# Kernel tuning notes

Measured on AMD Instinct MI355X. Metric: run time of the kernel, lower is better.

## Reference

```python
import jax, jax.numpy as jnp
import numpy as np

N = 10000        # nodes
E = 160000       # edges (before self loops)
F_IN = 4         # n_features
D = 128          # d_model (per-head out channels for GAT, GCN width)
H = 8            # n_heads
NEG_SLOPE = 0.2  # PyG GATConv default leaky relu slope


def setup_inputs() -> dict:
    key = jax.random.key(0)
    ks = jax.random.split(key, 10)
    x = jax.random.normal(ks[0], (N, F_IN), dtype=jnp.float32)
    edge_index = jax.random.randint(ks[1], (2, E), 0, N, dtype=jnp.int64)
    s = 0.05
    gat_w = jax.random.normal(ks[2], (F_IN, H * D), dtype=jnp.float32) * s
    att_src = jax.random.normal(ks[3], (H, D), dtype=jnp.float32) * s
    att_dst = jax.random.normal(ks[4], (H, D), dtype=jnp.float32) * s
    gat_b = jnp.zeros((H * D,), dtype=jnp.float32)
    gcn1_w = jax.random.normal(ks[5], (H * D, D), dtype=jnp.float32) * s
    gcn1_b = jnp.zeros((D,), dtype=jnp.float32)
    gcn2_w = jax.random.normal(ks[6], (D, D), dtype=jnp.float32) * s
    gcn2_b = jnp.zeros((D,), dtype=jnp.float32)
    return {"x": x, "edge_index": edge_index, "gat_w": gat_w,
            "att_src": att_src, "att_dst": att_dst, "gat_b": gat_b,
            "gcn1_w": gcn1_w, "gcn1_b": gcn1_b,
            "gcn2_w": gcn2_w, "gcn2_b": gcn2_b}


def _add_self_loops(edge_index, n):
    loops = jnp.arange(n, dtype=edge_index.dtype)
    src = jnp.concatenate([edge_index[0], loops])
    dst = jnp.concatenate([edge_index[1], loops])
    return src, dst


def _gat_conv(x, src, dst, w, att_src, att_dst, b):
    # PyG GATConv, concat=True: h [N,H,D]
    h = (x @ w).reshape(-1, H, D)
    a_s = jnp.einsum('nhd,hd->nh', h, att_src)   # per-node src score
    a_d = jnp.einsum('nhd,hd->nh', h, att_dst)   # per-node dst score
    e = jax.nn.leaky_relu(a_s[src] + a_d[dst], NEG_SLOPE)  # [Etot,H]
    # segment softmax over destination node, per head
    m = jax.ops.segment_max(e, dst, num_segments=N)
    ex = jnp.exp(e - m[dst])
    denom = jax.ops.segment_sum(ex, dst, num_segments=N)
    alpha = ex / denom[dst]                       # [Etot,H]
    msg = h[src] * alpha[:, :, None]              # [Etot,H,D]
    out = jax.ops.segment_sum(msg, dst, num_segments=N)  # [N,H,D]
    return out.reshape(-1, H * D) + b


def _gcn_conv(x, src, dst, w, b):
    # PyG GCNConv with symmetric normalization (self loops already added)
    h = x @ w
    deg = jax.ops.segment_sum(jnp.ones_like(dst, dtype=h.dtype), dst,
                              num_segments=N)
    dinv = jnp.where(deg > 0, jax.lax.rsqrt(deg), 0.0)
    norm = dinv[src] * dinv[dst]                  # [Etot]
    out = jax.ops.segment_sum(h[src] * norm[:, None], dst, num_segments=N)
    return out + b


def reference(x, edge_index, gat_w, att_src, att_dst, gat_b,
              gcn1_w, gcn1_b, gcn2_w, gcn2_b):
    src, dst = _add_self_loops(edge_index, N)
    h = _gat_conv(x, src, dst, gat_w, att_src, att_dst, gat_b)
    h = jax.nn.gelu(h, approximate=False)         # torch F.gelu is exact erf
    h = _gcn_conv(h, src, dst, gcn1_w, gcn1_b)
    h = jax.nn.gelu(h, approximate=False)
    h = _gcn_conv(h, src, dst, gcn2_w, gcn2_b)
    return h                                      # [N, D]
```

## Files before the change

kernel.cpp:

```cpp
#include <hip/hip_runtime.h>
#include <math.h>

#define HEADS 8
#define DHEAD 128
#define CMODEL 1024
#define BCAP 64

typedef __attribute__((ext_vector_type(8))) short bf16x8;
typedef __attribute__((ext_vector_type(4))) float f32x4;

__device__ __forceinline__ float gelu_exact(float x) {
    return 0.5f * x * (1.0f + erff(x * 0.70710678118654752440f));
}

__device__ __forceinline__ unsigned short f2bf(float f) {
    unsigned u = __float_as_uint(f);
    return (unsigned short)((u + 0x7FFFu + ((u >> 16) & 1u)) >> 16);
}
__device__ __forceinline__ float bf2f(unsigned short h) {
    return __uint_as_float((unsigned)h << 16);
}

__global__ void __launch_bounds__(256) k_scores(const float* __restrict__ x,
                                                const float* __restrict__ gat_w,
                                                const float* __restrict__ att_src,
                                                const float* __restrict__ att_dst,
                                                const float* __restrict__ W1,
                                                const float* __restrict__ W2,
                                                float* __restrict__ xpack,
                                                float* __restrict__ a_d,
                                                int* __restrict__ cursor,
                                                unsigned short* __restrict__ W1hi,
                                                unsigned short* __restrict__ W1lo,
                                                unsigned short* __restrict__ W2hi,
                                                unsigned short* __restrict__ W2lo,
                                                int n_nodes, int nb_scores) {
    if ((int)blockIdx.x >= nb_scores) {
        int t = (blockIdx.x - nb_scores) * 256 + threadIdx.x;
        const int total1 = (1024 >> 5) * 8 * 64;
        const int total2 = (128 >> 5) * 8 * 64;
        const float* W; unsigned short *Whi, *Wlo;
        if (t < total1) { W = W1; Whi = W1hi; Wlo = W1lo; }
        else if (t < total1 + total2) { t -= total1; W = W2; Whi = W2hi; Wlo = W2lo; }
        else return;
        int lane = t & 63;
        int ct = (t >> 6) & 7;
        int kc = t >> 9;
        int quad = lane >> 4;
        int col = ct * 16 + (lane & 15);
        size_t o = (size_t)t * 8;
        #pragma unroll
        for (int j = 0; j < 8; j++) {
            float w = W[(size_t)(kc * 32 + quad * 8 + j) * 128 + col];
            unsigned short h = f2bf(w);
            Whi[o + j] = h;
            Wlo[o + j] = f2bf(w - bf2f(h));
        }
        return;
    }
    __shared__ float ws_s[32], ws_d[32];
    int t = threadIdx.x;
    if (t < 64) {
        int e = t >> 1;
        int which = t & 1;
        int hh = e >> 2, k = e & 3;
        const float* wrow = gat_w + k * CMODEL + hh * DHEAD;
        const float* av = which ? (att_dst + hh * DHEAD) : (att_src + hh * DHEAD);
        float s = 0.0f;
        for (int c = 0; c < DHEAD; c++) s += wrow[c] * av[c];
        if (which) ws_d[e] = s; else ws_s[e] = s;
    }
    int gid = blockIdx.x * 256 + t;
    if (gid < n_nodes) cursor[gid] = 0;
    __syncthreads();
    int p = gid;
    if (p >= n_nodes * HEADS) return;
    int n = p >> 3, hh = p & 7;
    float4 xv = *(const float4*)(x + (size_t)n * 4);
    float4 ws = *(const float4*)&ws_s[hh * 4];
    float4 wd = *(const float4*)&ws_d[hh * 4];
    a_d[p] = xv.x * wd.x + xv.y * wd.y + xv.z * wd.z + xv.w * wd.w;
    xpack[(size_t)n * 16 + 4 + hh] =
        xv.x * ws.x + xv.y * ws.y + xv.z * ws.z + xv.w * ws.w;
    if (hh == 0) *(float4*)(xpack + (size_t)n * 16) = xv;
}

__global__ void __launch_bounds__(256) k_scatter(const int* __restrict__ ei,
                                                 int* __restrict__ cursor,
                                                 int* __restrict__ bucket,
                                                 int n_nodes, int n_edges) {
    int e = blockIdx.x * 256 + threadIdx.x;
    int etot = n_edges + n_nodes;
    if (e >= etot) return;
    int s, d;
    if (e < n_edges) { s = ei[e]; d = ei[n_edges + e]; }
    else             { s = d = e - n_edges; }
    int pos = atomicAdd(&cursor[d], 1);
    if (pos < BCAP) bucket[(d << 6) + pos] = s;
}

__global__ void __launch_bounds__(256, 3) k_smax_mm1(const float* __restrict__ xpack,
                                                  const float* __restrict__ a_d,
                                                  const int* __restrict__ deg,
                                                  const int* __restrict__ bucket,
                                                  const float* __restrict__ gat_w,
                                                  const float* __restrict__ gat_b,
                                                  const unsigned short* __restrict__ Bhi,
                                                  const unsigned short* __restrict__ Blo,
                                                  float* __restrict__ t,
                                                  int n_nodes) {
    __shared__ float xs[16 * 32];
    __shared__ float ck[2][16 * 68];
    int mb = blockIdx.x;
    int tid = threadIdx.x;
    int lane = tid & 63;
    int w = tid >> 6;

    bf16x8 bhA[2][2], blA[2][2], bhB[2][2], blB[2][2];
    #pragma unroll
    for (int kc2 = 0; kc2 < 2; kc2++)
        #pragma unroll
        for (int ct = 0; ct < 2; ct++) {
            size_t bi = (((size_t)(kc2 * 8) + w * 2 + ct) * 64 + lane) * 8;
            bhA[kc2][ct] = *(const bf16x8*)(Bhi + bi);
            blA[kc2][ct] = *(const bf16x8*)(Blo + bi);
        }

    {
        int q = tid >> 1;
        int half = tid & 1;
        int ln = tid >> 4, hh = q & 7;
        int n = mb * 16 + ln;
        int nc = (n < n_nodes) ? n : (n_nodes - 1);
        int grp = lane & 48;
        int gl = lane & 15;
        int basec = nc << 6;
        int pre0 = bucket[basec + gl];
        int pre1 = bucket[basec + 16 + gl];
        int pre2 = bucket[basec + 32 + gl];
        int pre3 = bucket[basec + 48 + gl];
        auto SRC = [&](int e) -> int {
            int v = (e < 16) ? pre0 : (e < 32) ? pre1 : (e < 48) ? pre2 : pre3;
            return __shfl(v, grp + (e & 15), 64);
        };
        float sum = 0.0f;
        float4 acc = make_float4(0, 0, 0, 0);
        if (n < n_nodes) {
            int dg = deg[n]; if (dg > BCAP) dg = BCAP;
            float ad = a_d[n * 8 + hh];
            int r = half;
            for (; r + 6 < dg; r += 8) {
                int s0 = SRC(r + 0), s1 = SRC(r + 2);
                int s2 = SRC(r + 4), s3 = SRC(r + 6);
                const float* p0 = xpack + (size_t)s0 * 16;
                const float* p1 = xpack + (size_t)s1 * 16;
                const float* p2 = xpack + (size_t)s2 * 16;
                const float* p3 = xpack + (size_t)s3 * 16;
                float e0 = p0[4 + hh] + ad, e1 = p1[4 + hh] + ad;
                float e2 = p2[4 + hh] + ad, e3 = p3[4 + hh] + ad;
                float4 x0 = *(const float4*)p0;
                float4 x1 = *(const float4*)p1;
                float4 x2 = *(const float4*)p2;
                float4 x3 = *(const float4*)p3;
                e0 = (e0 > 0.0f) ? e0 : 0.2f * e0;  float w0 = __expf(e0);
                e1 = (e1 > 0.0f) ? e1 : 0.2f * e1;  float w1 = __expf(e1);
                e2 = (e2 > 0.0f) ? e2 : 0.2f * e2;  float w2 = __expf(e2);
                e3 = (e3 > 0.0f) ? e3 : 0.2f * e3;  float w3 = __expf(e3);
                sum += w0 + w1 + w2 + w3;
                acc.x += w0 * x0.x + w1 * x1.x + w2 * x2.x + w3 * x3.x;
                acc.y += w0 * x0.y + w1 * x1.y + w2 * x2.y + w3 * x3.y;
                acc.z += w0 * x0.z + w1 * x1.z + w2 * x2.z + w3 * x3.z;
                acc.w += w0 * x0.w + w1 * x1.w + w2 * x2.w + w3 * x3.w;
            }
            for (; r < dg; r += 2) {
                int s = SRC(r);
                const float* ps = xpack + (size_t)s * 16;
                float e = ps[4 + hh] + ad;
                e = (e > 0.0f) ? e : 0.2f * e;
                float ex = __expf(e);
                float4 xv = *(const float4*)ps;
                sum += ex;
                acc.x += ex * xv.x; acc.y += ex * xv.y;
                acc.z += ex * xv.z; acc.w += ex * xv.w;
            }
        }
        sum   += __shfl_down(sum, 1);
        acc.x += __shfl_down(acc.x, 1);
        acc.y += __shfl_down(acc.y, 1);
        acc.z += __shfl_down(acc.z, 1);
        acc.w += __shfl_down(acc.w, 1);
        if (half == 0) {
            float inv = (sum > 0.0f) ? (1.0f / sum) : 0.0f;
            *(float4*)&xs[q * 4] = make_float4(acc.x * inv, acc.y * inv,
                                               acc.z * inv, acc.w * inv);
        }
    }
    __syncthreads();

    int lm = lane & 15, quad = lane >> 4;
    int cc = tid & 63;
    int rp = tid >> 6;
    f32x4 macc[2];
    macc[0] = (f32x4){0.0f, 0.0f, 0.0f, 0.0f};
    macc[1] = (f32x4){0.0f, 0.0f, 0.0f, 0.0f};

#define ROUND(RR, BH, BL, BH_N, BL_N, RNEXT)                                    \
    {                                                                           \
        int buf = (RR) & 1;                                                     \
        int col = (RR) * 64 + cc;                                               \
        float w0 = gat_w[col], w1 = gat_w[1024 + col],                          \
              w2 = gat_w[2048 + col], w3 = gat_w[3072 + col];                   \
        float bb = gat_b[col];                                                  \
        int hh2 = (RR) >> 1;                                                    \
        _Pragma("unroll")                                                       \
        for (int rr = 0; rr < 4; rr++) {                                        \
            int row = rp * 4 + rr;                                              \
            float4 xa = *(const float4*)&xs[(row * 8 + hh2) * 4];               \
            float v = xa.x * w0 + xa.y * w1 + xa.z * w2 + xa.w * w3 + bb;       \
            ck[buf][row * 68 + cc] = gelu_exact(v);                             \
        }                                                                       \
        _Pragma("unroll")                                                       \
        for (int kc2 = 0; kc2 < 2; kc2++)                                       \
            _Pragma("unroll")                                                   \
            for (int ct = 0; ct < 2; ct++) {                                    \
                size_t bi = (((size_t)((RNEXT) * 2 + kc2) * 8 + w * 2 + ct) * 64 + lane) * 8; \
                BH_N[kc2][ct] = *(const bf16x8*)(Bhi + bi);                     \
                BL_N[kc2][ct] = *(const bf16x8*)(Blo + bi);                     \
            }                                                                   \
        asm volatile("s_waitcnt lgkmcnt(0)" ::: "memory");                      \
        __builtin_amdgcn_s_barrier();                                           \
        __builtin_amdgcn_sched_barrier(0);                                      \
        _Pragma("unroll")                                                       \
        for (int kc2 = 0; kc2 < 2; kc2++) {                                     \
            float a[8];                                                         \
            *(float4*)&a[0] = *(const float4*)&ck[buf][lm * 68 + kc2 * 32 + quad * 8];     \
            *(float4*)&a[4] = *(const float4*)&ck[buf][lm * 68 + kc2 * 32 + quad * 8 + 4]; \
            bf16x8 ah, al;                                                      \
            _Pragma("unroll")                                                   \
            for (int j = 0; j < 8; j++) {                                       \
                unsigned short h = f2bf(a[j]);                                  \
                ah[j] = (short)h;                                               \
                al[j] = (short)f2bf(a[j] - bf2f(h));                            \
            }                                                                   \
            _Pragma("unroll")                                                   \
            for (int ct = 0; ct < 2; ct++) {                                    \
                macc[ct] = __builtin_amdgcn_mfma_f32_16x16x32_bf16(ah, BH[kc2][ct], macc[ct], 0, 0, 0); \
                macc[ct] = __builtin_amdgcn_mfma_f32_16x16x32_bf16(al, BH[kc2][ct], macc[ct], 0, 0, 0); \
                macc[ct] = __builtin_amdgcn_mfma_f32_16x16x32_bf16(ah, BL[kc2][ct], macc[ct], 0, 0, 0); \
            }                                                                   \
        }                                                                       \
    }

    for (int r = 0; r < 16; r += 2) {
        ROUND(r,     bhA, blA, bhB, blB, r + 1);
        ROUND(r + 1, bhB, blB, bhA, blA, (r + 2 < 16 ? r + 2 : 15));
    }
#undef ROUND

    #pragma unroll
    for (int ct = 0; ct < 2; ct++) {
        int col = (w * 2 + ct) * 16 + lm;
        #pragma unroll
        for (int reg = 0; reg < 4; reg++) {
            int row = mb * 16 + quad * 4 + reg;
            if (row < n_nodes) {
                float dv = 1.0f / sqrtf((float)deg[row]);
                t[(size_t)row * 128 + col] = macc[ct][reg] * dv;
            }
        }
    }
}

__global__ void __launch_bounds__(512) k_gcn1_fused(const float* __restrict__ t,
                                                    const int* __restrict__ deg,
                                                    const int* __restrict__ bucket,
                                                    const float* __restrict__ bias,
                                                    const unsigned short* __restrict__ Bhi,
                                                    const unsigned short* __restrict__ Blo,
                                                    float* __restrict__ t2,
                                                    int n_nodes) {
    __shared__ float hs[16][132];
    int tid = threadIdx.x;
    int mb = blockIdx.x;
    int c = tid & 31;
    int ln = tid >> 5;
    int node = mb * 16 + ln;
    int nc = (node < n_nodes) ? node : (n_nodes - 1);
    int base = nc << 6;
    int sa = bucket[base + c];
    int sb = bucket[base + 32 + c];
    int dgt = (node < n_nodes) ? deg[node] : 1;
    int dg = dgt > BCAP ? BCAP : dgt;
    float dn = 1.0f / sqrtf((float)dgt);
    int d1 = dg > 32 ? 32 : dg;
    #pragma unroll
    for (int h2 = 0; h2 < 2; h2++) {
        const float* tp = t + h2 * 64 + c * 2;
        float2 acc = make_float2(0.0f, 0.0f);
        int r = 0;
        for (; r + 4 <= d1; r += 4) {
            int s0 = __shfl(sa, r + 0, 32);
            int s1 = __shfl(sa, r + 1, 32);
            int s2 = __shfl(sa, r + 2, 32);
            int s3 = __shfl(sa, r + 3, 32);
            float2 v0 = *(const float2*)(tp + (size_t)s0 * 128);
            float2 v1 = *(const float2*)(tp + (size_t)s1 * 128);
            float2 v2 = *(const float2*)(tp + (size_t)s2 * 128);
            float2 v3 = *(const float2*)(tp + (size_t)s3 * 128);
            acc.x += v0.x + v1.x + v2.x + v3.x;
            acc.y += v0.y + v1.y + v2.y + v3.y;
        }
        for (; r < d1; r++) {
            int s = __shfl(sa, r, 32);
            float2 v = *(const float2*)(tp + (size_t)s * 128);
            acc.x += v.x; acc.y += v.y;
        }
        for (; r < dg; r++) {
            int s = __shfl(sb, r - 32, 32);
            float2 v = *(const float2*)(tp + (size_t)s * 128);
            acc.x += v.x; acc.y += v.y;
        }
        int k = h2 * 64 + c * 2;
        float2 bb = *(const float2*)(bias + k);
        hs[ln][k]     = gelu_exact(acc.x * dn + bb.x);
        hs[ln][k + 1] = gelu_exact(acc.y * dn + bb.y);
    }
    __syncthreads();
    int lane = tid & 63;
    int w = tid >> 6;
    int lm = lane & 15, quad = lane >> 4;
    f32x4 acc2 = (f32x4){0.0f, 0.0f, 0.0f, 0.0f};
    #pragma unroll
    for (int kc = 0; kc < 4; kc++) {
        float a[8];
        *(float4*)&a[0] = *(const float4*)&hs[lm][kc * 32 + quad * 8];
        *(float4*)&a[4] = *(const float4*)&hs[lm][kc * 32 + quad * 8 + 4];
        bf16x8 ah, al;
        #pragma unroll
        for (int j = 0; j < 8; j++) {
            unsigned short h = f2bf(a[j]);
            ah[j] = (short)h;
            al[j] = (short)f2bf(a[j] - bf2f(h));
        }
        bf16x8 bh = *(const bf16x8*)(Bhi + (((size_t)(kc * 8 + w)) * 64 + lane) * 8);
        bf16x8 bl = *(const bf16x8*)(Blo + (((size_t)(kc * 8 + w)) * 64 + lane) * 8);
        acc2 = __builtin_amdgcn_mfma_f32_16x16x32_bf16(ah, bh, acc2, 0, 0, 0);
        acc2 = __builtin_amdgcn_mfma_f32_16x16x32_bf16(al, bh, acc2, 0, 0, 0);
        acc2 = __builtin_amdgcn_mfma_f32_16x16x32_bf16(ah, bl, acc2, 0, 0, 0);
    }
    int col = w * 16 + lm;
    #pragma unroll
    for (int reg = 0; reg < 4; reg++) {
        int row = mb * 16 + quad * 4 + reg;
        if (row < n_nodes) {
            float dv = 1.0f / sqrtf((float)deg[row]);
            t2[(size_t)row * 128 + col] = acc2[reg] * dv;
        }
    }
}

__global__ void __launch_bounds__(256) k_gcn_agg(const float* __restrict__ t,
                                                 const int* __restrict__ deg,
                                                 const int* __restrict__ bucket,
                                                 const float* __restrict__ bias,
                                                 float* __restrict__ outF,
                                                 int n_nodes) {
    int c = threadIdx.x & 31;
    int ln = threadIdx.x >> 5;
    int n = blockIdx.x * 8 + ln;
    int col0 = blockIdx.y * 64;
    if (n >= n_nodes) return;
    float2 acc = make_float2(0.0f, 0.0f);
    int dgt = deg[n];
    int dg = dgt > BCAP ? BCAP : dgt;
    int base = n << 6;
    int sa = bucket[base + c];
    int sb = bucket[base + 32 + c];
    const float* tp = t + col0 + c * 2;
    int d1 = dg > 32 ? 32 : dg;
    int r = 0;
    for (; r + 4 <= d1; r += 4) {
        int s0 = __shfl(sa, r + 0, 32);
        int s1 = __shfl(sa, r + 1, 32);
        int s2 = __shfl(sa, r + 2, 32);
        int s3 = __shfl(sa, r + 3, 32);
        float2 v0 = *(const float2*)(tp + (size_t)s0 * 128);
        float2 v1 = *(const float2*)(tp + (size_t)s1 * 128);
        float2 v2 = *(const float2*)(tp + (size_t)s2 * 128);
        float2 v3 = *(const float2*)(tp + (size_t)s3 * 128);
        acc.x += v0.x + v1.x + v2.x + v3.x;
        acc.y += v0.y + v1.y + v2.y + v3.y;
    }
    for (; r < d1; r++) {
        int s = __shfl(sa, r, 32);
        float2 v = *(const float2*)(tp + (size_t)s * 128);
        acc.x += v.x; acc.y += v.y;
    }
    for (; r < dg; r++) {
        int s = __shfl(sb, r - 32, 32);
        float2 v = *(const float2*)(tp + (size_t)s * 128);
        acc.x += v.x; acc.y += v.y;
    }
    float dn = 1.0f / sqrtf((float)dgt);
    int k = col0 + c * 2;
    float2 bb = *(const float2*)(bias + k);
    *(float2*)(outF + (size_t)n * 128 + k) =
        make_float2(acc.x * dn + bb.x, acc.y * dn + bb.y);
}

extern "C" void kernel_launch(void* const* d_in, const int* in_sizes, int n_in,
                              void* d_out, int out_size, void* d_ws, size_t ws_size,
                              hipStream_t stream) {
    const float* x        = (const float*)d_in[0];
    const int*   ei       = (const int*)d_in[1];
    const float* gat_w    = (const float*)d_in[2];
    const float* att_src  = (const float*)d_in[3];
    const float* att_dst  = (const float*)d_in[4];
    const float* gat_b    = (const float*)d_in[5];
    const float* gcn1_w   = (const float*)d_in[6];
    const float* gcn1_b   = (const float*)d_in[7];
    const float* gcn2_w   = (const float*)d_in[8];
    const float* gcn2_b   = (const float*)d_in[9];
    float* out = (float*)d_out;

    int N = in_sizes[0] / 4;
    int E = in_sizes[1] / 2;
    int Etot = E + N;
    int n_mtiles = (N + 15) / 16;

    char* base = (char*)d_ws;
    float*          t      = (float*)(base);
    float*          t2     = (float*)(base + 5120000);
    unsigned short* w1hi   = (unsigned short*)(base + 26000000);
    unsigned short* w1lo   = (unsigned short*)(base + 26262144);
    unsigned short* w2hi   = (unsigned short*)(base + 26524288);
    unsigned short* w2lo   = (unsigned short*)(base + 26557056);
    size_t off = 81920000;
    float* xpack  = (float*)(base + off); off += (size_t)N * 16 * 4;
    float* a_d    = (float*)(base + off); off += (size_t)N * 8 * 4;
    int*   cursor = (int*)(base + off);   off += (size_t)N * 4;
    int*   bucket = (int*)(base + off);   off += (size_t)N * BCAP * 4;

    int nb_scores = (N * HEADS + 255) / 256;
    int nb_wswz   = (16384 + 2048 + 255) / 256;

    k_scores<<<nb_scores + nb_wswz, 256, 0, stream>>>(x, gat_w, att_src, att_dst,
                                                      gcn1_w, gcn2_w, xpack, a_d, cursor,
                                                      w1hi, w1lo, w2hi, w2lo, N, nb_scores);

    k_scatter<<<(Etot + 255) / 256, 256, 0, stream>>>(ei, cursor, bucket, N, E);

    k_smax_mm1<<<n_mtiles, 256, 0, stream>>>(xpack, a_d, cursor, bucket,
                                             gat_w, gat_b, w1hi, w1lo, t, N);

    k_gcn1_fused<<<n_mtiles, 512, 0, stream>>>(t, cursor, bucket, gcn1_b,
                                               w2hi, w2lo, t2, N);

    k_gcn_agg<<<dim3((N + 7) / 8, 2), 256, 0, stream>>>(t2, cursor, bucket, gcn2_b,
                                                        out, N);
}
```

Measured before the change: 153.1 us.

## Double k_smax_mm1 block to 512 threads, one column tile per wave

Changes the fused GAT softmax-aggregation plus GEMM kernel from 256 to 512 threads per block. Each wave now owns one 16-column MFMA tile instead of two, and four lanes instead of two split each node-head's edge loop, with an extra shuffle reduction. This cuts per-thread register pressure and serial work to raise occupancy and latency hiding. In exchange it adds shuffle overhead and larger-block barrier synchronisation.

```diff
diff --git a/kernel.cpp b/kernel.cpp
--- a/kernel.cpp
+++ b/kernel.cpp
@@ -99,7 +99,7 @@
     if (pos < BCAP) bucket[(d << 6) + pos] = s;
 }
 
-__global__ void __launch_bounds__(256, 3) k_smax_mm1(const float* __restrict__ xpack,
+__global__ void __launch_bounds__(512, 4) k_smax_mm1(const float* __restrict__ xpack,
                                                   const float* __restrict__ a_d,
                                                   const int* __restrict__ deg,
                                                   const int* __restrict__ bucket,
@@ -116,42 +116,38 @@
     int lane = tid & 63;
     int w = tid >> 6;
 
-    bf16x8 bhA[2][2], blA[2][2], bhB[2][2], blB[2][2];
+    bf16x8 bhA[2], blA[2], bhB[2], blB[2];
     #pragma unroll
-    for (int kc2 = 0; kc2 < 2; kc2++)
-        #pragma unroll
-        for (int ct = 0; ct < 2; ct++) {
-            size_t bi = (((size_t)(kc2 * 8) + w * 2 + ct) * 64 + lane) * 8;
-            bhA[kc2][ct] = *(const bf16x8*)(Bhi + bi);
-            blA[kc2][ct] = *(const bf16x8*)(Blo + bi);
-        }
+    for (int kc2 = 0; kc2 < 2; kc2++) {
+        size_t bi = (((size_t)kc2 * 8 + w) * 64 + lane) * 8;
+        bhA[kc2] = *(const bf16x8*)(Bhi + bi);
+        blA[kc2] = *(const bf16x8*)(Blo + bi);
+    }
 
     {
-        int q = tid >> 1;
-        int half = tid & 1;
-        int ln = tid >> 4, hh = q & 7;
+        int ln = tid >> 5;
+        int g = tid & 31;
+        int hh = g >> 2;
+        int quarter = g & 3;
         int n = mb * 16 + ln;
         int nc = (n < n_nodes) ? n : (n_nodes - 1);
-        int grp = lane & 48;
-        int gl = lane & 15;
         int basec = nc << 6;
-        int pre0 = bucket[basec + gl];
-        int pre1 = bucket[basec + 16 + gl];
-        int pre2 = bucket[basec + 32 + gl];
-        int pre3 = bucket[basec + 48 + gl];
+        int sa = bucket[basec + g];
+        int sb = bucket[basec + 32 + g];
+        int grp = lane & 32;
         auto SRC = [&](int e) -> int {
-            int v = (e < 16) ? pre0 : (e < 32) ? pre1 : (e < 48) ? pre2 : pre3;
-            return __shfl(v, grp + (e & 15), 64);
+            int v = (e < 32) ? sa : sb;
+            return __shfl(v, grp + (e & 31), 64);
         };
         float sum = 0.0f;
         float4 acc = make_float4(0, 0, 0, 0);
         if (n < n_nodes) {
             int dg = deg[n]; if (dg > BCAP) dg = BCAP;
             float ad = a_d[n * 8 + hh];
-            int r = half;
-            for (; r + 6 < dg; r += 8) {
-                int s0 = SRC(r + 0), s1 = SRC(r + 2);
-                int s2 = SRC(r + 4), s3 = SRC(r + 6);
+            int r = quarter;
+            for (; r + 12 < dg; r += 16) {
+                int s0 = SRC(r + 0), s1 = SRC(r + 4);
+                int s2 = SRC(r + 8), s3 = SRC(r + 12);
                 const float* p0 = xpack + (size_t)s0 * 16;
                 const float* p1 = xpack + (size_t)s1 * 16;
                 const float* p2 = xpack + (size_t)s2 * 16;
@@ -172,7 +168,7 @@
                 acc.z += w0 * x0.z + w1 * x1.z + w2 * x2.z + w3 * x3.z;
                 acc.w += w0 * x0.w + w1 * x1.w + w2 * x2.w + w3 * x3.w;
             }
-            for (; r < dg; r += 2) {
+            for (; r < dg; r += 4) {
                 int s = SRC(r);
                 const float* ps = xpack + (size_t)s * 16;
                 float e = ps[4 + hh] + ad;
@@ -189,10 +185,15 @@
         acc.y += __shfl_down(acc.y, 1);
         acc.z += __shfl_down(acc.z, 1);
         acc.w += __shfl_down(acc.w, 1);
-        if (half == 0) {
+        sum   += __shfl_down(sum, 2);
+        acc.x += __shfl_down(acc.x, 2);
+        acc.y += __shfl_down(acc.y, 2);
+        acc.z += __shfl_down(acc.z, 2);
+        acc.w += __shfl_down(acc.w, 2);
+        if (quarter == 0) {
             float inv = (sum > 0.0f) ? (1.0f / sum) : 0.0f;
-            *(float4*)&xs[q * 4] = make_float4(acc.x * inv, acc.y * inv,
-                                               acc.z * inv, acc.w * inv);
+            *(float4*)&xs[(ln * 8 + hh) * 4] = make_float4(acc.x * inv, acc.y * inv,
+                                                           acc.z * inv, acc.w * inv);
         }
     }
     __syncthreads();
@@ -200,9 +201,7 @@
     int lm = lane & 15, quad = lane >> 4;
     int cc = tid & 63;
     int rp = tid >> 6;
-    f32x4 macc[2];
-    macc[0] = (f32x4){0.0f, 0.0f, 0.0f, 0.0f};
-    macc[1] = (f32x4){0.0f, 0.0f, 0.0f, 0.0f};
+    f32x4 macc = (f32x4){0.0f, 0.0f, 0.0f, 0.0f};
 
 #define ROUND(RR, BH, BL, BH_N, BL_N, RNEXT)                                    \
     {                                                                           \
@@ -213,20 +212,18 @@
         float bb = gat_b[col];                                                  \
         int hh2 = (RR) >> 1;                                                    \
         _Pragma("unroll")                                                       \
-        for (int rr = 0; rr < 4; rr++) {                                        \
-            int row = rp * 4 + rr;                                              \
+        for (int rr = 0; rr < 2; rr++) {                                        \
+            int row = rp * 2 + rr;                                              \
             float4 xa = *(const float4*)&xs[(row * 8 + hh2) * 4];               \
             float v = xa.x * w0 + xa.y * w1 + xa.z * w2 + xa.w * w3 + bb;       \
             ck[buf][row * 68 + cc] = gelu_exact(v);                             \
         }                                                                       \
         _Pragma("unroll")                                                       \
-        for (int kc2 = 0; kc2 < 2; kc2++)                                       \
-            _Pragma("unroll")                                                   \
-            for (int ct = 0; ct < 2; ct++) {                                    \
-                size_t bi = (((size_t)((RNEXT) * 2 + kc2) * 8 + w * 2 + ct) * 64 + lane) * 8; \
-                BH_N[kc2][ct] = *(const bf16x8*)(Bhi + bi);                     \
-                BL_N[kc2][ct] = *(const bf16x8*)(Blo + bi);                     \
-            }                                                                   \
+        for (int kc2 = 0; kc2 < 2; kc2++) {                                     \
+            size_t bi = (((size_t)((RNEXT) * 2 + kc2) * 8 + w) * 64 + lane) * 8;\
+            BH_N[kc2] = *(const bf16x8*)(Bhi + bi);                             \
+            BL_N[kc2] = *(const bf16x8*)(Blo + bi);                             \
+        }                                                                       \
         asm volatile("s_waitcnt lgkmcnt(0)" ::: "memory");                      \
         __builtin_amdgcn_s_barrier();                                           \
         __builtin_amdgcn_sched_barrier(0);                                      \
@@ -242,12 +239,9 @@
                 ah[j] = (short)h;                                               \
                 al[j] = (short)f2bf(a[j] - bf2f(h));                            \
             }                                                                   \
-            _Pragma("unroll")                                                   \
-            for (int ct = 0; ct < 2; ct++) {                                    \
-                macc[ct] = __builtin_amdgcn_mfma_f32_16x16x32_bf16(ah, BH[kc2][ct], macc[ct], 0, 0, 0); \
-                macc[ct] = __builtin_amdgcn_mfma_f32_16x16x32_bf16(al, BH[kc2][ct], macc[ct], 0, 0, 0); \
-                macc[ct] = __builtin_amdgcn_mfma_f32_16x16x32_bf16(ah, BL[kc2][ct], macc[ct], 0, 0, 0); \
-            }                                                                   \
+            macc = __builtin_amdgcn_mfma_f32_16x16x32_bf16(ah, BH[kc2], macc, 0, 0, 0); \
+            macc = __builtin_amdgcn_mfma_f32_16x16x32_bf16(al, BH[kc2], macc, 0, 0, 0); \
+            macc = __builtin_amdgcn_mfma_f32_16x16x32_bf16(ah, BL[kc2], macc, 0, 0, 0); \
         }                                                                       \
     }
 
@@ -257,15 +251,14 @@
     }
 #undef ROUND
 
-    #pragma unroll
-    for (int ct = 0; ct < 2; ct++) {
-        int col = (w * 2 + ct) * 16 + lm;
+    {
+        int col = w * 16 + lm;
         #pragma unroll
         for (int reg = 0; reg < 4; reg++) {
             int row = mb * 16 + quad * 4 + reg;
             if (row < n_nodes) {
                 float dv = 1.0f / sqrtf((float)deg[row]);
-                t[(size_t)row * 128 + col] = macc[ct][reg] * dv;
+                t[(size_t)row * 128 + col] = macc[reg] * dv;
             }
         }
     }
@@ -450,7 +443,7 @@
 
     k_scatter<<<(Etot + 255) / 256, 256, 0, stream>>>(ei, cursor, bucket, N, E);
 
-    k_smax_mm1<<<n_mtiles, 256, 0, stream>>>(xpack, a_d, cursor, bucket,
+    k_smax_mm1<<<n_mtiles, 512, 0, stream>>>(xpack, a_d, cursor, bucket,
                                              gat_w, gat_b, w1hi, w1lo, t, N);
 
     k_gcn1_fused<<<n_mtiles, 512, 0, stream>>>(t, cursor, bucket, gcn1_b,
```

Result: slower. 162.0 us (+5.8%).

## Split GEMM K-dimension across waves with LDS reduction in smax_mm1

Applied to the files above, without the earlier changes.

Replaces the column-split MFMA loop, which staged GELU activations through a double-buffered LDS tile with a barrier every round, with a split-K scheme. Each wave computes GELU activations for its own K slices directly in registers and accumulates all 128 output columns. The four partial sums are then reduced through shared memory before the scaled write. This removes the 16 per-round barriers and the LDS round trip for activations, but needs more accumulator registers. The launch-bounds occupancy hint is dropped and a serial reduction by one wave is added.

```diff
diff --git a/kernel.cpp b/kernel.cpp
--- a/kernel.cpp
+++ b/kernel.cpp
@@ -99,7 +99,7 @@
     if (pos < BCAP) bucket[(d << 6) + pos] = s;
 }
 
-__global__ void __launch_bounds__(256, 3) k_smax_mm1(const float* __restrict__ xpack,
+__global__ void __launch_bounds__(256) k_smax_mm1(const float* __restrict__ xpack,
                                                   const float* __restrict__ a_d,
                                                   const int* __restrict__ deg,
                                                   const int* __restrict__ bucket,
@@ -110,21 +110,11 @@
                                                   float* __restrict__ t,
                                                   int n_nodes) {
     __shared__ float xs[16 * 32];
-    __shared__ float ck[2][16 * 68];
+    __shared__ float red[3][64][36];
     int mb = blockIdx.x;
     int tid = threadIdx.x;
     int lane = tid & 63;
     int w = tid >> 6;
-
-    bf16x8 bhA[2][2], blA[2][2], bhB[2][2], blB[2][2];
-    #pragma unroll
-    for (int kc2 = 0; kc2 < 2; kc2++)
-        #pragma unroll
-        for (int ct = 0; ct < 2; ct++) {
-            size_t bi = (((size_t)(kc2 * 8) + w * 2 + ct) * 64 + lane) * 8;
-            bhA[kc2][ct] = *(const bf16x8*)(Bhi + bi);
-            blA[kc2][ct] = *(const bf16x8*)(Blo + bi);
-        }
 
     {
         int q = tid >> 1;
@@ -198,74 +188,71 @@
     __syncthreads();
 
     int lm = lane & 15, quad = lane >> 4;
-    int cc = tid & 63;
-    int rp = tid >> 6;
-    f32x4 macc[2];
-    macc[0] = (f32x4){0.0f, 0.0f, 0.0f, 0.0f};
-    macc[1] = (f32x4){0.0f, 0.0f, 0.0f, 0.0f};
-
-#define ROUND(RR, BH, BL, BH_N, BL_N, RNEXT)                                    \
-    {                                                                           \
-        int buf = (RR) & 1;                                                     \
-        int col = (RR) * 64 + cc;                                               \
-        float w0 = gat_w[col], w1 = gat_w[1024 + col],                          \
-              w2 = gat_w[2048 + col], w3 = gat_w[3072 + col];                   \
-        float bb = gat_b[col];                                                  \
-        int hh2 = (RR) >> 1;                                                    \
-        _Pragma("unroll")                                                       \
-        for (int rr = 0; rr < 4; rr++) {                                        \
-            int row = rp * 4 + rr;                                              \
-            float4 xa = *(const float4*)&xs[(row * 8 + hh2) * 4];               \
-            float v = xa.x * w0 + xa.y * w1 + xa.z * w2 + xa.w * w3 + bb;       \
-            ck[buf][row * 68 + cc] = gelu_exact(v);                             \
-        }                                                                       \
-        _Pragma("unroll")                                                       \
-        for (int kc2 = 0; kc2 < 2; kc2++)                                       \
-            _Pragma("unroll")                                                   \
-            for (int ct = 0; ct < 2; ct++) {                                    \
-                size_t bi = (((size_t)((RNEXT) * 2 + kc2) * 8 + w * 2 + ct) * 64 + lane) * 8; \
-                BH_N[kc2][ct] = *(const bf16x8*)(Bhi + bi);                     \
-                BL_N[kc2][ct] = *(const bf16x8*)(Blo + bi);                     \
-            }                                                                   \
-        asm volatile("s_waitcnt lgkmcnt(0)" ::: "memory");                      \
-        __builtin_amdgcn_s_barrier();                                           \
-        __builtin_amdgcn_sched_barrier(0);                                      \
-        _Pragma("unroll")                                                       \
-        for (int kc2 = 0; kc2 < 2; kc2++) {                                     \
-            float a[8];                                                         \
-            *(float4*)&a[0] = *(const float4*)&ck[buf][lm * 68 + kc2 * 32 + quad * 8];     \
-            *(float4*)&a[4] = *(const float4*)&ck[buf][lm * 68 + kc2 * 32 + quad * 8 + 4]; \
-            bf16x8 ah, al;                                                      \
-            _Pragma("unroll")                                                   \
-            for (int j = 0; j < 8; j++) {                                       \
-                unsigned short h = f2bf(a[j]);                                  \
-                ah[j] = (short)h;                                               \
-                al[j] = (short)f2bf(a[j] - bf2f(h));                            \
-            }                                                                   \
-            _Pragma("unroll")                                                   \
-            for (int ct = 0; ct < 2; ct++) {                                    \
-                macc[ct] = __builtin_amdgcn_mfma_f32_16x16x32_bf16(ah, BH[kc2][ct], macc[ct], 0, 0, 0); \
-                macc[ct] = __builtin_amdgcn_mfma_f32_16x16x32_bf16(al, BH[kc2][ct], macc[ct], 0, 0, 0); \
-                macc[ct] = __builtin_amdgcn_mfma_f32_16x16x32_bf16(ah, BL[kc2][ct], macc[ct], 0, 0, 0); \
-            }                                                                   \
-        }                                                                       \
-    }
-
-    for (int r = 0; r < 16; r += 2) {
-        ROUND(r,     bhA, blA, bhB, blB, r + 1);
-        ROUND(r + 1, bhB, blB, bhA, blA, (r + 2 < 16 ? r + 2 : 15));
-    }
-#undef ROUND
-
+    f32x4 acc[8];
     #pragma unroll
-    for (int ct = 0; ct < 2; ct++) {
-        int col = (w * 2 + ct) * 16 + lm;
-        #pragma unroll
-        for (int reg = 0; reg < 4; reg++) {
-            int row = mb * 16 + quad * 4 + reg;
-            if (row < n_nodes) {
-                float dv = 1.0f / sqrtf((float)deg[row]);
-                t[(size_t)row * 128 + col] = macc[ct][reg] * dv;
+    for (int ct = 0; ct < 8; ct++) acc[ct] = (f32x4){0.0f, 0.0f, 0.0f, 0.0f};
+
+    #pragma unroll 2
+    for (int s = 0; s < 8; s++) {
+        int kc = w * 8 + s;
+        int hh2 = kc >> 2;
+        int col0 = kc * 32 + quad * 8;
+        float wrf[4][8];
+        float bbf[8];
+        #pragma unroll
+        for (int j4 = 0; j4 < 4; j4++) {
+            *(float4*)&wrf[j4][0] = *(const float4*)(gat_w + j4 * 1024 + col0);
+            *(float4*)&wrf[j4][4] = *(const float4*)(gat_w + j4 * 1024 + col0 + 4);
+        }
+        *(float4*)&bbf[0] = *(const float4*)(gat_b + col0);
+        *(float4*)&bbf[4] = *(const float4*)(gat_b + col0 + 4);
+        float4 xa = *(const float4*)&xs[(lm * 8 + hh2) * 4];
+        bf16x8 ah, al;
+        #pragma unroll
+        for (int j = 0; j < 8; j++) {
+            float v = xa.x * wrf[0][j] + xa.y * wrf[1][j]
+                    + xa.z * wrf[2][j] + xa.w * wrf[3][j] + bbf[j];
+            v = gelu_exact(v);
+            unsigned short h = f2bf(v);
+            ah[j] = (short)h;
+            al[j] = (short)f2bf(v - bf2f(h));
+        }
+        #pragma unroll
+        for (int ct = 0; ct < 8; ct++) {
+            size_t bi = (((size_t)(kc * 8 + ct)) * 64 + lane) * 8;
+            bf16x8 bh = *(const bf16x8*)(Bhi + bi);
+            bf16x8 bl = *(const bf16x8*)(Blo + bi);
+            acc[ct] = __builtin_amdgcn_mfma_f32_16x16x32_bf16(ah, bh, acc[ct], 0, 0, 0);
+            acc[ct] = __builtin_amdgcn_mfma_f32_16x16x32_bf16(al, bh, acc[ct], 0, 0, 0);
+            acc[ct] = __builtin_amdgcn_mfma_f32_16x16x32_bf16(ah, bl, acc[ct], 0, 0, 0);
+        }
+    }
+
+    if (w > 0) {
+        #pragma unroll
+        for (int ct = 0; ct < 8; ct++)
+            *(f32x4*)&red[w - 1][lane][ct * 4] = acc[ct];
+    }
+    __syncthreads();
+    if (w == 0) {
+        #pragma unroll
+        for (int v = 0; v < 3; v++)
+            #pragma unroll
+            for (int ct = 0; ct < 8; ct++) {
+                float4 r = *(const float4*)&red[v][lane][ct * 4];
+                acc[ct][0] += r.x; acc[ct][1] += r.y;
+                acc[ct][2] += r.z; acc[ct][3] += r.w;
+            }
+        #pragma unroll
+        for (int ct = 0; ct < 8; ct++) {
+            int col = ct * 16 + lm;
+            #pragma unroll
+            for (int reg = 0; reg < 4; reg++) {
+                int row = mb * 16 + quad * 4 + reg;
+                if (row < n_nodes) {
+                    float dv = 1.0f / sqrtf((float)deg[row]);
+                    t[(size_t)row * 128 + col] = acc[ct][reg] * dv;
+                }
             }
         }
     }
```

After: 186.9 us. 22.1% more time.
